# Optimization experiments

Measured on AMD Instinct MI355X. Metric: run time of the kernel, lower is better.

Reference implementation:

```python
import jax, jax.numpy as jnp
import numpy as np

B, CIN, T, H, W = 2, 512, 8, 32, 32
COUT = 512

def conv2d(x, w, b):
    # x: (B, C, H, W), w: (O, I, kh, kw) -> (B, O, H, W), SAME padding
    y = jax.lax.conv_general_dilated(x, w, (1, 1), 'SAME',
        dimension_numbers=('NCHW', 'OIHW', 'NCHW'))
    return y + b[None, :, None, None]

def convlstm(x, w, b, wci, wcf, wco):
    # x: (B, C, T, H, W) -> (B, Cout, T, H, W); peepholes wci/wcf/wco: (Cout, H, W)
    bb, c, t, hh, ww = x.shape
    cout = wci.shape[0]
    h0 = jnp.zeros((bb, cout, hh, ww), x.dtype)

    def step(carry, xt):
        Hp, Cp = carry
        z = conv2d(jnp.concatenate([xt, Hp], axis=1), w, b)  # (B, 4*Cout, H, W)
        ic, fc, cc, oc = jnp.split(z, 4, axis=1)
        i = jax.nn.sigmoid(ic + wci * Cp)
        f = jax.nn.sigmoid(fc + wcf * Cp)
        Cn = f * Cp + i * jax.nn.relu(cc)   # activation='relu'
        o = jax.nn.sigmoid(oc + wco * Cn)
        Hn = o * jax.nn.relu(Cn)
        return (Hn, Cn), Hn

    (_, _), hs = jax.lax.scan(step, (h0, h0), jnp.moveaxis(x, 2, 0))
    return jnp.moveaxis(hs, 0, 2)  # (B, Cout, T, H, W)

def setup_inputs():
    key = jax.random.key(0)
    ks = jax.random.split(key, 16)
    inp = {'x': jax.random.normal(ks[0], (B, CIN, T, H, W), jnp.float32)}
    for l in range(3):
        k = ks[1 + 5 * l: 6 + 5 * l]
        inp['conv_w%d' % (l + 1)] = jax.random.normal(k[0], (4 * COUT, CIN + COUT, 3, 3), jnp.float32) * 0.02
        inp['conv_b%d' % (l + 1)] = jnp.zeros((4 * COUT,), jnp.float32)
        inp['wci%d' % (l + 1)] = jax.random.normal(k[1], (COUT, H, W), jnp.float32) * 0.02
        inp['wcf%d' % (l + 1)] = jax.random.normal(k[2], (COUT, H, W), jnp.float32) * 0.02
        inp['wco%d' % (l + 1)] = jax.random.normal(k[3], (COUT, H, W), jnp.float32) * 0.02
    return inp

def reference(x, conv_w1, conv_b1, wci1, wcf1, wco1,
              conv_w2, conv_b2, wci2, wcf2, wco2,
              conv_w3, conv_b3, wci3, wcf3, wco3):
    y = convlstm(x, conv_w1, conv_b1, wci1, wcf1, wco1)
    y = convlstm(y, conv_w2, conv_b2, wci2, wcf2, wco2)
    y = convlstm(y, conv_w3, conv_b3, wci3, wcf3, wco3)
    # Sigmoid on last time step: output[:, :, -1] -> (B, Cout, H, W)
    return jax.nn.sigmoid(y[:, :, -1])
```

## Files before the change

kernel.cpp:

```cpp
#include <hip/hip_runtime.h>

typedef unsigned short u16;
typedef __bf16 bf16x8 __attribute__((ext_vector_type(8)));
typedef float f32x4 __attribute__((ext_vector_type(4)));

#define T_STEPS 8
#define PLANE 1156
#define ROWB 2176

__device__ __forceinline__ u16 f2bf(float f) {
    unsigned u = __float_as_uint(f);
    return (u16)((u + 0x7fff + ((u >> 16) & 1)) >> 16);
}
__device__ __forceinline__ float sigmoidf(float x) {
    return 1.f / (1.f + expf(-x));
}
__device__ __forceinline__ void gl_lds16(const void* g, void* l) {
    __builtin_amdgcn_global_load_lds(
        (const __attribute__((address_space(1))) void*)g,
        (__attribute__((address_space(3))) void*)l, 16, 0, 0);
}

__global__ __launch_bounds__(256) void repack_w(const float* __restrict__ w,
                         u16* __restrict__ wx, u16* __restrict__ wh) {
    __shared__ u16 L[128][150];
    const int tid = threadIdx.x;
    const int bidx = blockIdx.x;
    const int part   = bidx >> 9;
    const int co_blk = (bidx >> 5) & 15;
    const int cc     = (bidx >> 1) & 15;
    const int half   = bidx & 1;
    const int cibase = part * 512 + cc * 32 + half * 16;

#pragma unroll
    for (int k = 0; k < 18; ++k) {
        int i = tid + k * 256;
        int co_in = i / 36;
        int p4 = i - co_in * 36;
        int co = part ? ((co_in & 3) * 512 + co_blk * 32 + (co_in >> 2))
                      : (co_blk * 128 + co_in);
        const float4 v = *(const float4*)(w + (size_t)co * 9216
                                            + (size_t)cibase * 9 + p4 * 4);
        L[co_in][p4 * 4 + 0] = f2bf(v.x);
        L[co_in][p4 * 4 + 1] = f2bf(v.y);
        L[co_in][p4 * 4 + 2] = f2bf(v.z);
        L[co_in][p4 * 4 + 3] = f2bf(v.w);
    }
    __syncthreads();
    u16* wout = part ? wh : wx;
#pragma unroll
    for (int k = 0; k < 9; ++k) {
        int v2 = tid + k * 256;
        int co_in = v2 & 127;
        int rq = v2 >> 7;
        int q01 = rq >= 9;
        int r = rq - q01 * 9;
        int quad = half * 2 + q01;
        union { u16 u[8]; uint4 q; } tmp;
#pragma unroll
        for (int j = 0; j < 8; ++j)
            tmp.u[j] = L[co_in][(q01 * 8 + j) * 9 + r];
        *(uint4*)(wout + ((((size_t)co_blk * 144 + cc * 9 + r) * 4 + quad) * 128
                          + co_in) * 8) = tmp.q;
    }
}

__global__ __launch_bounds__(256) void pretransform_x(
    const float* __restrict__ x, u16* __restrict__ Xp) {
    const int bt = blockIdx.x >> 5;
    const int y  = blockIdx.x & 31;
    const int b  = bt >> 3;
    const int xx = threadIdx.x & 31, cg0 = threadIdx.x >> 5;
    const float* src = x + ((size_t)(b * 512) * T_STEPS + (bt & 7)) * 1024
                         + y * 32 + xx;
    u16* dst = Xp + (((size_t)bt * 34 + y + 1) * 34 + (xx + 1)) * 512;
#pragma unroll
    for (int it = 0; it < 8; ++it) {
        const int cig = cg0 + it * 8;
        union { u16 u[8]; uint4 v; } pk;
#pragma unroll
        for (int j = 0; j < 8; ++j)
            pk.u[j] = f2bf(src[(size_t)(cig * 8 + j) * 8192]);
        *(uint4*)(dst + cig * 8) = pk.v;
    }
}

#define READB4(dstv, btcp, rr) {                                             \
    const int ry_ = (rr) / 3, rx_ = (rr) % 3;                                \
    dstv[0] = *(const bf16x8*)((btcp) + wnrow + (0 + ry_) * ROWB + colb[0][rx_]); \
    dstv[1] = *(const bf16x8*)((btcp) + wnrow + (0 + ry_) * ROWB + colb[1][rx_]); \
    dstv[2] = *(const bf16x8*)((btcp) + wnrow + (1 + ry_) * ROWB + colb[0][rx_]); \
    dstv[3] = *(const bf16x8*)((btcp) + wnrow + (1 + ry_) * ROWB + colb[1][rx_]); }

#define READB2(dstv, btcp, rr) {                                             \
    const int ry_ = (rr) / 3, rx_ = (rr) % 3;                                \
    dstv[0] = *(const bf16x8*)((btcp) + wnrow + ry_ * ROWB + colb[0][rx_]);  \
    dstv[1] = *(const bf16x8*)((btcp) + wnrow + ry_ * ROWB + colb[1][rx_]); }

__global__ __launch_bounds__(512, 4) void conv_gemm(
    const u16* __restrict__ Wp, const u16* __restrict__ Xp, int t0,
    float* __restrict__ Z) {
    __shared__ __align__(16) u16 Bt[2][6528];

    const int tid = threadIdx.x;
    const int bid = blockIdx.y * 32 + blockIdx.x;
    const int swz = (bid & 7) * 64 + (bid >> 3);
    const int co_blk = swz >> 5;
    const int nblk   = swz & 31;
    const int n0 = nblk * 128;

    const int wave = tid >> 6, lane = tid & 63;
    const int wm = wave >> 1, wn = wave & 1;
    const int q_l = lane >> 4, m_l = lane & 15;

    const int plane = n0 >> 10;
    const int bb_ = plane & 1;
    const int tt  = t0 + (plane >> 1);
    const int pyb = (n0 & 1023) >> 5;
    const u16* pbase = Xp + (size_t)(bb_ * T_STEPS + tt) * PLANE * 512;

    const int c0 = tid;
    const int p0 = c0 >> 2, sl0 = c0 & 3;
    const int yl0 = p0 / 34, xl0 = p0 - yl0 * 34;
    const int src0 = ((pyb + yl0) * 34 + xl0) * 512 + ((sl0 ^ ((xl0 >> 1) & 3)) << 3);
    const int c1 = 512 + tid;
    const int p1 = c1 >> 2, sl1 = c1 & 3;
    const int yl1 = p1 / 34, xl1 = p1 - yl1 * 34;
    const int src1 = ((pyb + yl1) * 34 + xl1) * 512 + ((sl1 ^ ((xl1 >> 1) & 3)) << 3);
    const bool do1 = tid < 304;

    const uint4* Aq = (const uint4*)Wp + (size_t)co_blk * 144 * 512
                      + q_l * 128 + wm * 32 + m_l;

    int colb[2][3];
#pragma unroll
    for (int xh = 0; xh < 2; xh++)
#pragma unroll
        for (int rx = 0; rx < 3; rx++) {
            int xl = xh * 16 + m_l + rx;
            colb[xh][rx] = xl * 64 + ((q_l ^ ((xl >> 1) & 3)) << 4);
        }
    const int wnrow = wn * 2 * ROWB;

    f32x4 acc[2][4];
#pragma unroll
    for (int i = 0; i < 2; i++)
#pragma unroll
        for (int j = 0; j < 4; j++) acc[i][j] = (f32x4){0.f, 0.f, 0.f, 0.f};

    bf16x8 areg[3][2], breg[2][4];

    gl_lds16(pbase + src0, &Bt[0][c0 * 8]);
    if (do1) gl_lds16(pbase + src1, &Bt[0][c1 * 8]);
#pragma unroll
    for (int mt = 0; mt < 2; ++mt) {
        areg[0][mt] = *(const bf16x8*)(Aq + mt * 16);
        areg[1][mt] = *(const bf16x8*)(Aq + 512 + mt * 16);
    }

    for (int cc = 0; cc < 16; ++cc) {
        const int cb = cc & 1;
        const char* btc = (const char*)&Bt[cb][0];
        asm volatile("" ::: "memory");
        if (cc == 0) asm volatile("s_waitcnt vmcnt(4)" ::: "memory");
        else         asm volatile("s_waitcnt vmcnt(14)" ::: "memory");
        __builtin_amdgcn_s_barrier();
        asm volatile("" ::: "memory");
        READB4(breg[0], btc, 0);
#pragma unroll
        for (int r = 0; r < 9; ++r) {
            const int kt = cc * 9 + r;
            if (cc < 15 || r < 7) {
#pragma unroll
                for (int mt = 0; mt < 2; ++mt)
                    areg[(r + 2) % 3][mt] =
                        *(const bf16x8*)(Aq + (size_t)(kt + 2) * 512 + mt * 16);
            }
            if (r == 1 && cc < 15) {
                const u16* gs = pbase + (cc + 1) * 32;
                gl_lds16(gs + src0, &Bt[cb ^ 1][c0 * 8]);
                if (do1) gl_lds16(gs + src1, &Bt[cb ^ 1][c1 * 8]);
            }
            if (r < 8) READB4(breg[(r + 1) & 1], btc, (r + 1));
            __builtin_amdgcn_s_setprio(1);
#pragma unroll
            for (int mt = 0; mt < 2; ++mt)
#pragma unroll
                for (int nt = 0; nt < 4; ++nt)
                    acc[mt][nt] = __builtin_amdgcn_mfma_f32_16x16x32_bf16(
                        areg[r % 3][mt], breg[r & 1][nt], acc[mt][nt], 0, 0, 0);
            __builtin_amdgcn_s_setprio(0);
        }
    }

#pragma unroll
    for (int mt = 0; mt < 2; mt++)
#pragma unroll
        for (int nt = 0; nt < 4; nt++)
#pragma unroll
            for (int reg = 0; reg < 4; reg++) {
                int co = co_blk * 128 + wm * 32 + mt * 16 + q_l * 4 + reg;
                int n  = n0 + wn * 64 + nt * 16 + m_l;
                Z[(size_t)co * 4096 + n] = acc[mt][nt][reg];
            }
}

__global__ __launch_bounds__(512, 4) void hconv_gates(
    const u16* __restrict__ Wp, const u16* __restrict__ Yprev, int tprev,
    const float* __restrict__ zx, int nxoff,
    const float* __restrict__ bias,
    const float* __restrict__ wci, const float* __restrict__ wcf,
    const float* __restrict__ wco,
    float* __restrict__ C, u16* __restrict__ Yp, int t,
    float* __restrict__ outp) {
    __shared__ __align__(16) u16 Bt[2][4352];

    const int tid = threadIdx.x;
    const int bid = blockIdx.y * 32 + blockIdx.x;
    const int swz = (bid & 7) * 64 + (bid >> 3);
    const int co_blk = swz >> 5;
    const int nblk   = swz & 31;
    const int n0 = nblk * 64;

    const int wave = tid >> 6, lane = tid & 63;
    const int wm = wave >> 1, wn = wave & 1;
    const int q_l = lane >> 4, m_l = lane & 15;

    const int b = n0 >> 10;
    const int pyb = (n0 & 1023) >> 5;
    const u16* pbase = Yprev + (size_t)(b * T_STEPS + tprev) * PLANE * 512;

    const int p0 = tid >> 2, sl0 = tid & 3;
    const int yl0 = p0 / 34, xl0 = p0 - yl0 * 34;
    const int src0 = ((pyb + yl0) * 34 + xl0) * 512 + ((sl0 ^ ((xl0 >> 1) & 3)) << 3);
    const int c1 = 512 + tid;
    const int p1 = c1 >> 2, sl1 = c1 & 3;
    const int yl1 = p1 / 34, xl1 = p1 - yl1 * 34;
    const int src1 = ((pyb + yl1) * 34 + xl1) * 512 + ((sl1 ^ ((xl1 >> 1) & 3)) << 3);
    const bool do1 = tid < 32;

    const uint4* Aq = (const uint4*)Wp + (size_t)co_blk * 144 * 512
                      + q_l * 128 + wm * 32 + m_l;

    int colb[2][3];
#pragma unroll
    for (int nt = 0; nt < 2; nt++)
#pragma unroll
        for (int rx = 0; rx < 3; rx++) {
            int xl = nt * 16 + m_l + rx;
            colb[nt][rx] = xl * 64 + ((q_l ^ ((xl >> 1) & 3)) << 4);
        }
    const int wnrow = wn * ROWB;

    f32x4 acc[2][2];
#pragma unroll
    for (int i = 0; i < 2; i++)
#pragma unroll
        for (int j = 0; j < 2; j++) acc[i][j] = (f32x4){0.f, 0.f, 0.f, 0.f};

    bf16x8 areg[3][2], breg[2][2];

    gl_lds16(pbase + src0, &Bt[0][tid * 8]);
    if (do1) gl_lds16(pbase + src1, &Bt[0][c1 * 8]);
#pragma unroll
    for (int mt = 0; mt < 2; ++mt) {
        areg[0][mt] = *(const bf16x8*)(Aq + mt * 16);
        areg[1][mt] = *(const bf16x8*)(Aq + 512 + mt * 16);
    }

    for (int cc = 0; cc < 16; ++cc) {
        const int cb = cc & 1;
        const char* btc = (const char*)&Bt[cb][0];
        asm volatile("" ::: "memory");
        if (cc == 0) asm volatile("s_waitcnt vmcnt(4)" ::: "memory");
        else         asm volatile("s_waitcnt vmcnt(14)" ::: "memory");
        __builtin_amdgcn_s_barrier();
        asm volatile("" ::: "memory");
        READB2(breg[0], btc, 0);
#pragma unroll
        for (int r = 0; r < 9; ++r) {
            const int kt = cc * 9 + r;
            if (cc < 15 || r < 7) {
#pragma unroll
                for (int mt = 0; mt < 2; ++mt)
                    areg[(r + 2) % 3][mt] =
                        *(const bf16x8*)(Aq + (size_t)(kt + 2) * 512 + mt * 16);
            }
            if (r == 1 && cc < 15) {
                const u16* gs = pbase + (cc + 1) * 32;
                gl_lds16(gs + src0, &Bt[cb ^ 1][tid * 8]);
                if (do1) gl_lds16(gs + src1, &Bt[cb ^ 1][c1 * 8]);
            }
            if (r < 8) READB2(breg[(r + 1) & 1], btc, (r + 1));
            __builtin_amdgcn_s_setprio(1);
#pragma unroll
            for (int mt = 0; mt < 2; ++mt)
#pragma unroll
                for (int nt = 0; nt < 2; ++nt)
                    acc[mt][nt] = __builtin_amdgcn_mfma_f32_16x16x32_bf16(
                        areg[r % 3][mt], breg[r & 1][nt], acc[mt][nt], 0, 0, 0);
            __builtin_amdgcn_s_setprio(0);
        }
    }

#pragma unroll
    for (int mt = 0; mt < 2; ++mt) {
        const int ch = co_blk * 32 + wm * 8 + mt * 4 + q_l;
#pragma unroll
        for (int nt = 0; nt < 2; ++nt) {
            const int n = n0 + wn * 32 + nt * 16 + m_l;
            const int s = n & 1023;
            const int zcol = nxoff + n;
            float zi = acc[mt][nt][0] + zx[(size_t)ch * 4096 + zcol]          + bias[ch];
            float zf = acc[mt][nt][1] + zx[(size_t)(512 + ch) * 4096 + zcol]  + bias[512 + ch];
            float zc = acc[mt][nt][2] + zx[(size_t)(1024 + ch) * 4096 + zcol] + bias[1024 + ch];
            float zo = acc[mt][nt][3] + zx[(size_t)(1536 + ch) * 4096 + zcol] + bias[1536 + ch];
            const size_t ci_ = (size_t)(b * 512 + ch) * 1024 + s;
            const int ps = ch * 1024 + s;
            float Cp = C[ci_];
            float gi = sigmoidf(zi + wci[ps] * Cp);
            float gf = sigmoidf(zf + wcf[ps] * Cp);
            float Cn = gf * Cp + gi * fmaxf(zc, 0.f);
            float go = sigmoidf(zo + wco[ps] * Cn);
            float Hn = go * fmaxf(Cn, 0.f);
            C[ci_] = Cn;
            const int yp = (s >> 5) + 1, xp = (s & 31) + 1;
            Yp[(((size_t)(b * T_STEPS + t) * 34 + yp) * 34 + xp) * 512 + ch] = f2bf(Hn);
            if (outp) outp[ci_] = sigmoidf(Hn);
        }
    }
}

__global__ __launch_bounds__(256) void gates_kernel(
    const float* __restrict__ zx, int nxoff,
    const float* __restrict__ bias,
    const float* __restrict__ wci, const float* __restrict__ wcf,
    const float* __restrict__ wco,
    float* __restrict__ C, int is_first,
    u16* __restrict__ Yp, int t,
    float* __restrict__ outp) {
    __shared__ u16 Hs[16][136];
    const int tid = threadIdx.x;
    const int s0  = blockIdx.x * 128;
    const int co0 = blockIdx.y * 16;
    const int b   = blockIdx.z;
    const int sl = tid & 127, ch = tid >> 7;
    const int s = s0 + sl;

#pragma unroll
    for (int k = 0; k < 8; ++k) {
        const int co = co0 + k * 2 + ch;
        const size_t zi_ = (size_t)co * 4096 + nxoff + b * 1024 + s;
        float zi = zx[zi_]                       + bias[co];
        float zf = zx[zi_ + (size_t)512 * 4096]  + bias[co + 512];
        float zc = zx[zi_ + (size_t)1024 * 4096] + bias[co + 1024];
        float zo = zx[zi_ + (size_t)1536 * 4096] + bias[co + 1536];
        const size_t ci_ = ((size_t)b * 512 + co) * 1024 + s;
        float Cp = is_first ? 0.f : C[ci_];
        const int ps = co * 1024 + s;
        float gi = sigmoidf(zi + wci[ps] * Cp);
        float gf = sigmoidf(zf + wcf[ps] * Cp);
        float Cn = gf * Cp + gi * fmaxf(zc, 0.f);
        float go = sigmoidf(zo + wco[ps] * Cn);
        float Hn = go * fmaxf(Cn, 0.f);
        C[ci_] = Cn;
        Hs[k * 2 + ch][sl] = f2bf(Hn);
        if (outp) outp[ci_] = sigmoidf(Hn);
    }
    __syncthreads();
    const int sl2 = tid & 127, half = tid >> 7;
    const int s2 = s0 + sl2;
    const int yp = (s2 >> 5) + 1, xp = (s2 & 31) + 1;
    u16* dst = Yp + (((size_t)(b * T_STEPS + t) * 34 + yp) * 34 + xp) * 512
                  + co0 + half * 8;
    union { u16 u[8]; uint4 v; } pk;
#pragma unroll
    for (int j = 0; j < 8; ++j) pk.u[j] = Hs[half * 8 + j][sl2];
    *(uint4*)dst = pk.v;
}

extern "C" void kernel_launch(void* const* d_in, const int* in_sizes, int n_in,
                              void* d_out, int out_size, void* d_ws, size_t ws_size,
                              hipStream_t stream) {
    const float* x = (const float*)d_in[0];

    char* ws = (char*)d_ws;
    size_t off = 0;
    auto carve = [&](size_t bytes) { char* p = ws + off; off += (bytes + 255) & ~(size_t)255; return p; };

    u16*   Wx   = (u16*)  carve((size_t)16 * 144 * 4096 * 2);
    u16*   Wh   = (u16*)  carve((size_t)16 * 144 * 4096 * 2);
    float* Zx   = (float*)carve((size_t)2048 * 4096 * 4);
    float* Cbuf = (float*)carve((size_t)2 * 512 * 1024 * 4);
    const size_t PADB = (size_t)16 * PLANE * 512 * 2;
    u16*   Yp1  = (u16*)  carve(PADB);
    u16*   Yp2  = (u16*)  carve(PADB);
    (void)ws_size; (void)in_sizes; (void)n_in; (void)out_size;

    hipMemsetAsync(Yp1, 0, PADB, stream);
    hipMemsetAsync(Yp2, 0, PADB, stream);
    pretransform_x<<<512, 256, 0, stream>>>(x, Yp2);

    for (int l = 0; l < 3; ++l) {
        const float* w    = (const float*)d_in[1 + 5 * l];
        const float* bias = (const float*)d_in[2 + 5 * l];
        const float* wci  = (const float*)d_in[3 + 5 * l];
        const float* wcf  = (const float*)d_in[4 + 5 * l];
        const float* wco  = (const float*)d_in[5 + 5 * l];
        const u16* inl = (l == 0) ? Yp2 : (l == 1 ? Yp1 : Yp2);
        u16* Ycur      = (l == 0) ? Yp1 : (l == 1 ? Yp2 : Yp1);

        repack_w<<<1024, 256, 0, stream>>>(w, Wx, Wh);

        for (int t = 0; t < T_STEPS; ++t) {
            if ((t & 1) == 0)
                conv_gemm<<<dim3(32, 16), 512, 0, stream>>>(Wx, inl, t, Zx);
            float* outp = (l == 2 && t == T_STEPS - 1) ? (float*)d_out : nullptr;
            if (t == 0) {
                gates_kernel<<<dim3(8, 32, 2), 256, 0, stream>>>(
                    Zx, 0, bias, wci, wcf, wco, Cbuf, 1, Ycur, 0, outp);
            } else {
                hconv_gates<<<dim3(32, 16), 512, 0, stream>>>(
                    Wh, Ycur, t - 1, Zx, (t & 1) * 2048,
                    bias, wci, wcf, wco, Cbuf, Ycur, t, outp);
            }
        }
    }
}
```

Baseline: 2.075 ms.

## Deepen LDS B-fragment prefetch, unroll chunk pairs, and stage H stores through LDS

Both conv kernels now prefetch B fragments two taps ahead using a triple-buffered register set, and drop the s_setprio toggles. The 16-chunk loop is unrolled in pairs so the LDS buffer index is a compile-time constant. The gate epilogue writes bf16 H into a shared tile and then emits coalesced 16-byte stores per pixel, replacing scattered 2-byte stores. This adds register pressure and an extra barrier.

Result: slower. 2.134 ms (+2.8%).

```diff
diff --git a/kernel.cpp b/kernel.cpp
--- a/kernel.cpp
+++ b/kernel.cpp
@@ -97,6 +97,76 @@
     dstv[0] = *(const bf16x8*)((btcp) + wnrow + ry_ * ROWB + colb[0][rx_]);  \
     dstv[1] = *(const bf16x8*)((btcp) + wnrow + ry_ * ROWB + colb[1][rx_]); }
 
+#define XCHUNK(ccv, CBV)                                                      \
+{                                                                             \
+    const int cc_ = (ccv);                                                    \
+    const char* btc = (const char*)&Bt[CBV][0];                               \
+    asm volatile("" ::: "memory");                                            \
+    if (cc_ == 0) asm volatile("s_waitcnt vmcnt(4)" ::: "memory");            \
+    else          asm volatile("s_waitcnt vmcnt(14)" ::: "memory");           \
+    __builtin_amdgcn_s_barrier();                                             \
+    asm volatile("" ::: "memory");                                            \
+    READB4(breg[0], btc, 0);                                                  \
+    READB4(breg[1], btc, 1);                                                  \
+    _Pragma("unroll")                                                         \
+    for (int r = 0; r < 9; ++r) {                                             \
+        const int kt_ = cc_ * 9 + r;                                          \
+        if (cc_ < 15 || r < 7) {                                              \
+            _Pragma("unroll")                                                 \
+            for (int mt = 0; mt < 2; ++mt)                                    \
+                areg[(r + 2) % 3][mt] =                                       \
+                    *(const bf16x8*)(Aq + (size_t)(kt_ + 2) * 512 + mt * 16); \
+        }                                                                     \
+        if (r == 1 && cc_ < 15) {                                             \
+            const u16* gs = pbase + (cc_ + 1) * 32;                           \
+            gl_lds16(gs + src0, &Bt[(CBV) ^ 1][c0 * 8]);                      \
+            if (do1) gl_lds16(gs + src1, &Bt[(CBV) ^ 1][c1 * 8]);             \
+        }                                                                     \
+        if (r < 7) READB4(breg[(r + 2) % 3], btc, r + 2);                     \
+        _Pragma("unroll")                                                     \
+        for (int mt = 0; mt < 2; ++mt)                                        \
+            _Pragma("unroll")                                                 \
+            for (int nt = 0; nt < 4; ++nt)                                    \
+                acc[mt][nt] = __builtin_amdgcn_mfma_f32_16x16x32_bf16(        \
+                    areg[r % 3][mt], breg[r % 3][nt], acc[mt][nt], 0, 0, 0);  \
+    }                                                                         \
+}
+
+#define HCHUNK(ccv, CBV)                                                      \
+{                                                                             \
+    const int cc_ = (ccv);                                                    \
+    const char* btc = (const char*)&Bt[CBV][0];                               \
+    asm volatile("" ::: "memory");                                            \
+    if (cc_ == 0) asm volatile("s_waitcnt vmcnt(4)" ::: "memory");            \
+    else          asm volatile("s_waitcnt vmcnt(14)" ::: "memory");           \
+    __builtin_amdgcn_s_barrier();                                             \
+    asm volatile("" ::: "memory");                                            \
+    READB2(breg[0], btc, 0);                                                  \
+    READB2(breg[1], btc, 1);                                                  \
+    _Pragma("unroll")                                                         \
+    for (int r = 0; r < 9; ++r) {                                             \
+        const int kt_ = cc_ * 9 + r;                                          \
+        if (cc_ < 15 || r < 7) {                                              \
+            _Pragma("unroll")                                                 \
+            for (int mt = 0; mt < 2; ++mt)                                    \
+                areg[(r + 2) % 3][mt] =                                       \
+                    *(const bf16x8*)(Aq + (size_t)(kt_ + 2) * 512 + mt * 16); \
+        }                                                                     \
+        if (r == 1 && cc_ < 15) {                                             \
+            const u16* gs = pbase + (cc_ + 1) * 32;                           \
+            gl_lds16(gs + src0, &Bt[(CBV) ^ 1][tid * 8]);                     \
+            if (do1) gl_lds16(gs + src1, &Bt[(CBV) ^ 1][c1 * 8]);             \
+        }                                                                     \
+        if (r < 7) READB2(breg[(r + 2) % 3], btc, r + 2);                     \
+        _Pragma("unroll")                                                     \
+        for (int mt = 0; mt < 2; ++mt)                                        \
+            _Pragma("unroll")                                                 \
+            for (int nt = 0; nt < 2; ++nt)                                    \
+                acc[mt][nt] = __builtin_amdgcn_mfma_f32_16x16x32_bf16(        \
+                    areg[r % 3][mt], breg[r % 3][nt], acc[mt][nt], 0, 0, 0);  \
+    }                                                                         \
+}
+
 __global__ __launch_bounds__(512, 4) void conv_gemm(
     const u16* __restrict__ Wp, const u16* __restrict__ Xp, int t0,
     float* __restrict__ Z) {
@@ -148,7 +218,7 @@
 #pragma unroll
         for (int j = 0; j < 4; j++) acc[i][j] = (f32x4){0.f, 0.f, 0.f, 0.f};
 
-    bf16x8 areg[3][2], breg[2][4];
+    bf16x8 areg[3][2], breg[3][4];
 
     gl_lds16(pbase + src0, &Bt[0][c0 * 8]);
     if (do1) gl_lds16(pbase + src1, &Bt[0][c1 * 8]);
@@ -158,40 +228,13 @@
         areg[1][mt] = *(const bf16x8*)(Aq + 512 + mt * 16);
     }
 
-    for (int cc = 0; cc < 16; ++cc) {
-        const int cb = cc & 1;
-        const char* btc = (const char*)&Bt[cb][0];
-        asm volatile("" ::: "memory");
-        if (cc == 0) asm volatile("s_waitcnt vmcnt(4)" ::: "memory");
-        else         asm volatile("s_waitcnt vmcnt(14)" ::: "memory");
-        __builtin_amdgcn_s_barrier();
-        asm volatile("" ::: "memory");
-        READB4(breg[0], btc, 0);
-#pragma unroll
-        for (int r = 0; r < 9; ++r) {
-            const int kt = cc * 9 + r;
-            if (cc < 15 || r < 7) {
-#pragma unroll
-                for (int mt = 0; mt < 2; ++mt)
-                    areg[(r + 2) % 3][mt] =
-                        *(const bf16x8*)(Aq + (size_t)(kt + 2) * 512 + mt * 16);
-            }
-            if (r == 1 && cc < 15) {
-                const u16* gs = pbase + (cc + 1) * 32;
-                gl_lds16(gs + src0, &Bt[cb ^ 1][c0 * 8]);
-                if (do1) gl_lds16(gs + src1, &Bt[cb ^ 1][c1 * 8]);
-            }
-            if (r < 8) READB4(breg[(r + 1) & 1], btc, (r + 1));
-            __builtin_amdgcn_s_setprio(1);
-#pragma unroll
-            for (int mt = 0; mt < 2; ++mt)
-#pragma unroll
-                for (int nt = 0; nt < 4; ++nt)
-                    acc[mt][nt] = __builtin_amdgcn_mfma_f32_16x16x32_bf16(
-                        areg[r % 3][mt], breg[r & 1][nt], acc[mt][nt], 0, 0, 0);
-            __builtin_amdgcn_s_setprio(0);
-        }
-    }
+    XCHUNK(0, 0);
+#pragma unroll 1
+    for (int cch = 0; cch < 7; ++cch) {
+        XCHUNK(2 * cch + 1, 1);
+        XCHUNK(2 * cch + 2, 0);
+    }
+    XCHUNK(15, 1);
 
 #pragma unroll
     for (int mt = 0; mt < 2; mt++)
@@ -214,6 +257,7 @@
     float* __restrict__ C, u16* __restrict__ Yp, int t,
     float* __restrict__ outp) {
     __shared__ __align__(16) u16 Bt[2][4352];
+    __shared__ u16 Hs[32][66];
 
     const int tid = threadIdx.x;
     const int bid = blockIdx.y * 32 + blockIdx.x;
@@ -258,7 +302,7 @@
 #pragma unroll
         for (int j = 0; j < 2; j++) acc[i][j] = (f32x4){0.f, 0.f, 0.f, 0.f};
 
-    bf16x8 areg[3][2], breg[2][2];
+    bf16x8 areg[3][2], breg[3][2];
 
     gl_lds16(pbase + src0, &Bt[0][tid * 8]);
     if (do1) gl_lds16(pbase + src1, &Bt[0][c1 * 8]);
@@ -268,47 +312,22 @@
         areg[1][mt] = *(const bf16x8*)(Aq + 512 + mt * 16);
     }
 
-    for (int cc = 0; cc < 16; ++cc) {
-        const int cb = cc & 1;
-        const char* btc = (const char*)&Bt[cb][0];
-        asm volatile("" ::: "memory");
-        if (cc == 0) asm volatile("s_waitcnt vmcnt(4)" ::: "memory");
-        else         asm volatile("s_waitcnt vmcnt(14)" ::: "memory");
-        __builtin_amdgcn_s_barrier();
-        asm volatile("" ::: "memory");
-        READB2(breg[0], btc, 0);
-#pragma unroll
-        for (int r = 0; r < 9; ++r) {
-            const int kt = cc * 9 + r;
-            if (cc < 15 || r < 7) {
-#pragma unroll
-                for (int mt = 0; mt < 2; ++mt)
-                    areg[(r + 2) % 3][mt] =
-                        *(const bf16x8*)(Aq + (size_t)(kt + 2) * 512 + mt * 16);
-            }
-            if (r == 1 && cc < 15) {
-                const u16* gs = pbase + (cc + 1) * 32;
-                gl_lds16(gs + src0, &Bt[cb ^ 1][tid * 8]);
-                if (do1) gl_lds16(gs + src1, &Bt[cb ^ 1][c1 * 8]);
-            }
-            if (r < 8) READB2(breg[(r + 1) & 1], btc, (r + 1));
-            __builtin_amdgcn_s_setprio(1);
-#pragma unroll
-            for (int mt = 0; mt < 2; ++mt)
-#pragma unroll
-                for (int nt = 0; nt < 2; ++nt)
-                    acc[mt][nt] = __builtin_amdgcn_mfma_f32_16x16x32_bf16(
-                        areg[r % 3][mt], breg[r & 1][nt], acc[mt][nt], 0, 0, 0);
-            __builtin_amdgcn_s_setprio(0);
-        }
-    }
+    HCHUNK(0, 0);
+#pragma unroll 1
+    for (int cch = 0; cch < 7; ++cch) {
+        HCHUNK(2 * cch + 1, 1);
+        HCHUNK(2 * cch + 2, 0);
+    }
+    HCHUNK(15, 1);
 
 #pragma unroll
     for (int mt = 0; mt < 2; ++mt) {
-        const int ch = co_blk * 32 + wm * 8 + mt * 4 + q_l;
+        const int chl = wm * 8 + mt * 4 + q_l;
+        const int ch = co_blk * 32 + chl;
 #pragma unroll
         for (int nt = 0; nt < 2; ++nt) {
-            const int n = n0 + wn * 32 + nt * 16 + m_l;
+            const int nloc = wn * 32 + nt * 16 + m_l;
+            const int n = n0 + nloc;
             const int s = n & 1023;
             const int zcol = nxoff + n;
             float zi = acc[mt][nt][0] + zx[(size_t)ch * 4096 + zcol]          + bias[ch];
@@ -324,10 +343,20 @@
             float go = sigmoidf(zo + wco[ps] * Cn);
             float Hn = go * fmaxf(Cn, 0.f);
             C[ci_] = Cn;
-            const int yp = (s >> 5) + 1, xp = (s & 31) + 1;
-            Yp[(((size_t)(b * T_STEPS + t) * 34 + yp) * 34 + xp) * 512 + ch] = f2bf(Hn);
+            Hs[chl][nloc] = f2bf(Hn);
             if (outp) outp[ci_] = sigmoidf(Hn);
         }
+    }
+    __syncthreads();
+    if (tid < 256) {
+        const int nl = tid >> 2, cp = (tid & 3) << 3;
+        const int s = (n0 & 1023) + nl;
+        u16* yd = Yp + (((size_t)(b * T_STEPS + t) * 34 + (s >> 5) + 1) * 34
+                        + (s & 31) + 1) * 512 + co_blk * 32 + cp;
+        union { u16 u[8]; uint4 v; } pk;
+#pragma unroll
+        for (int j = 0; j < 8; ++j) pk.u[j] = Hs[cp + j][nl];
+        *(uint4*)yd = pk.v;
     }
 }
 
```

## Fuse input conv GEMM into recurrent step launch to overlap with hidden conv

Applied to the files above, without the earlier changes.

Merges the input-side conv GEMM and the recurrent hconv+gates kernel into one lstm_step kernel, selecting the role by blockIdx.z. The input conv blocks for future timesteps now run in the same launch as the recurrent work for the current step, so they can fill CUs left idle by the small recurrent grid. To make this safe the Z buffer becomes a three-slot ring (LDZ=6144 columns). The t=0 gates kernel is also simplified to drop the zero-valued cell-state terms. The cost is higher register and LDS pressure from a kernel with two branches, and contention between the two roles for bandwidth.

Measured after the change: 2.050 ms. About the same (-1.2%).

```diff
diff --git a/kernel.cpp b/kernel.cpp
--- a/kernel.cpp
+++ b/kernel.cpp
@@ -7,6 +7,7 @@
 #define T_STEPS 8
 #define PLANE 1156
 #define ROWB 2176
+#define LDZ 6144
 
 __device__ __forceinline__ u16 f2bf(float f) {
     unsigned u = __float_as_uint(f);
@@ -97,246 +98,243 @@
     dstv[0] = *(const bf16x8*)((btcp) + wnrow + ry_ * ROWB + colb[0][rx_]);  \
     dstv[1] = *(const bf16x8*)((btcp) + wnrow + ry_ * ROWB + colb[1][rx_]); }
 
-__global__ __launch_bounds__(512, 4) void conv_gemm(
-    const u16* __restrict__ Wp, const u16* __restrict__ Xp, int t0,
-    float* __restrict__ Z) {
-    __shared__ __align__(16) u16 Bt[2][6528];
-
-    const int tid = threadIdx.x;
-    const int bid = blockIdx.y * 32 + blockIdx.x;
-    const int swz = (bid & 7) * 64 + (bid >> 3);
-    const int co_blk = swz >> 5;
-    const int nblk   = swz & 31;
-    const int n0 = nblk * 128;
-
-    const int wave = tid >> 6, lane = tid & 63;
-    const int wm = wave >> 1, wn = wave & 1;
-    const int q_l = lane >> 4, m_l = lane & 15;
-
-    const int plane = n0 >> 10;
-    const int bb_ = plane & 1;
-    const int tt  = t0 + (plane >> 1);
-    const int pyb = (n0 & 1023) >> 5;
-    const u16* pbase = Xp + (size_t)(bb_ * T_STEPS + tt) * PLANE * 512;
-
-    const int c0 = tid;
-    const int p0 = c0 >> 2, sl0 = c0 & 3;
-    const int yl0 = p0 / 34, xl0 = p0 - yl0 * 34;
-    const int src0 = ((pyb + yl0) * 34 + xl0) * 512 + ((sl0 ^ ((xl0 >> 1) & 3)) << 3);
-    const int c1 = 512 + tid;
-    const int p1 = c1 >> 2, sl1 = c1 & 3;
-    const int yl1 = p1 / 34, xl1 = p1 - yl1 * 34;
-    const int src1 = ((pyb + yl1) * 34 + xl1) * 512 + ((sl1 ^ ((xl1 >> 1) & 3)) << 3);
-    const bool do1 = tid < 304;
-
-    const uint4* Aq = (const uint4*)Wp + (size_t)co_blk * 144 * 512
-                      + q_l * 128 + wm * 32 + m_l;
-
-    int colb[2][3];
-#pragma unroll
-    for (int xh = 0; xh < 2; xh++)
-#pragma unroll
-        for (int rx = 0; rx < 3; rx++) {
-            int xl = xh * 16 + m_l + rx;
-            colb[xh][rx] = xl * 64 + ((q_l ^ ((xl >> 1) & 3)) << 4);
-        }
-    const int wnrow = wn * 2 * ROWB;
-
-    f32x4 acc[2][4];
-#pragma unroll
-    for (int i = 0; i < 2; i++)
-#pragma unroll
-        for (int j = 0; j < 4; j++) acc[i][j] = (f32x4){0.f, 0.f, 0.f, 0.f};
-
-    bf16x8 areg[3][2], breg[2][4];
-
-    gl_lds16(pbase + src0, &Bt[0][c0 * 8]);
-    if (do1) gl_lds16(pbase + src1, &Bt[0][c1 * 8]);
-#pragma unroll
-    for (int mt = 0; mt < 2; ++mt) {
-        areg[0][mt] = *(const bf16x8*)(Aq + mt * 16);
-        areg[1][mt] = *(const bf16x8*)(Aq + 512 + mt * 16);
-    }
-
-    for (int cc = 0; cc < 16; ++cc) {
-        const int cb = cc & 1;
-        const char* btc = (const char*)&Bt[cb][0];
-        asm volatile("" ::: "memory");
-        if (cc == 0) asm volatile("s_waitcnt vmcnt(4)" ::: "memory");
-        else         asm volatile("s_waitcnt vmcnt(14)" ::: "memory");
-        __builtin_amdgcn_s_barrier();
-        asm volatile("" ::: "memory");
-        READB4(breg[0], btc, 0);
-#pragma unroll
-        for (int r = 0; r < 9; ++r) {
-            const int kt = cc * 9 + r;
-            if (cc < 15 || r < 7) {
-#pragma unroll
-                for (int mt = 0; mt < 2; ++mt)
-                    areg[(r + 2) % 3][mt] =
-                        *(const bf16x8*)(Aq + (size_t)(kt + 2) * 512 + mt * 16);
-            }
-            if (r == 1 && cc < 15) {
-                const u16* gs = pbase + (cc + 1) * 32;
-                gl_lds16(gs + src0, &Bt[cb ^ 1][c0 * 8]);
-                if (do1) gl_lds16(gs + src1, &Bt[cb ^ 1][c1 * 8]);
-            }
-            if (r < 8) READB4(breg[(r + 1) & 1], btc, (r + 1));
-            __builtin_amdgcn_s_setprio(1);
-#pragma unroll
-            for (int mt = 0; mt < 2; ++mt)
-#pragma unroll
-                for (int nt = 0; nt < 4; ++nt)
-                    acc[mt][nt] = __builtin_amdgcn_mfma_f32_16x16x32_bf16(
-                        areg[r % 3][mt], breg[r & 1][nt], acc[mt][nt], 0, 0, 0);
-            __builtin_amdgcn_s_setprio(0);
-        }
-    }
-
-#pragma unroll
-    for (int mt = 0; mt < 2; mt++)
-#pragma unroll
-        for (int nt = 0; nt < 4; nt++)
-#pragma unroll
-            for (int reg = 0; reg < 4; reg++) {
-                int co = co_blk * 128 + wm * 32 + mt * 16 + q_l * 4 + reg;
-                int n  = n0 + wn * 64 + nt * 16 + m_l;
-                Z[(size_t)co * 4096 + n] = acc[mt][nt][reg];
-            }
-}
-
-__global__ __launch_bounds__(512, 4) void hconv_gates(
-    const u16* __restrict__ Wp, const u16* __restrict__ Yprev, int tprev,
-    const float* __restrict__ zx, int nxoff,
+__global__ __launch_bounds__(512, 4) void lstm_step(
+    const u16* __restrict__ Wx, const u16* __restrict__ Wh,
+    const u16* __restrict__ Xp, const u16* __restrict__ Yprev,
+    int t0x, int zoffA, int zoffB,
+    int tprev, int zoffH,
     const float* __restrict__ bias,
     const float* __restrict__ wci, const float* __restrict__ wcf,
     const float* __restrict__ wco,
     float* __restrict__ C, u16* __restrict__ Yp, int t,
-    float* __restrict__ outp) {
-    __shared__ __align__(16) u16 Bt[2][4352];
+    float* __restrict__ outp,
+    float* __restrict__ Z, int role0) {
+    __shared__ __align__(16) char smem[26112];
 
     const int tid = threadIdx.x;
-    const int bid = blockIdx.y * 32 + blockIdx.x;
-    const int swz = (bid & 7) * 64 + (bid >> 3);
-    const int co_blk = swz >> 5;
-    const int nblk   = swz & 31;
-    const int n0 = nblk * 64;
-
     const int wave = tid >> 6, lane = tid & 63;
     const int wm = wave >> 1, wn = wave & 1;
     const int q_l = lane >> 4, m_l = lane & 15;
-
-    const int b = n0 >> 10;
-    const int pyb = (n0 & 1023) >> 5;
-    const u16* pbase = Yprev + (size_t)(b * T_STEPS + tprev) * PLANE * 512;
-
-    const int p0 = tid >> 2, sl0 = tid & 3;
-    const int yl0 = p0 / 34, xl0 = p0 - yl0 * 34;
-    const int src0 = ((pyb + yl0) * 34 + xl0) * 512 + ((sl0 ^ ((xl0 >> 1) & 3)) << 3);
-    const int c1 = 512 + tid;
-    const int p1 = c1 >> 2, sl1 = c1 & 3;
-    const int yl1 = p1 / 34, xl1 = p1 - yl1 * 34;
-    const int src1 = ((pyb + yl1) * 34 + xl1) * 512 + ((sl1 ^ ((xl1 >> 1) & 3)) << 3);
-    const bool do1 = tid < 32;
-
-    const uint4* Aq = (const uint4*)Wp + (size_t)co_blk * 144 * 512
-                      + q_l * 128 + wm * 32 + m_l;
-
-    int colb[2][3];
-#pragma unroll
-    for (int nt = 0; nt < 2; nt++)
-#pragma unroll
-        for (int rx = 0; rx < 3; rx++) {
-            int xl = nt * 16 + m_l + rx;
-            colb[nt][rx] = xl * 64 + ((q_l ^ ((xl >> 1) & 3)) << 4);
-        }
-    const int wnrow = wn * ROWB;
-
-    f32x4 acc[2][2];
-#pragma unroll
-    for (int i = 0; i < 2; i++)
-#pragma unroll
-        for (int j = 0; j < 2; j++) acc[i][j] = (f32x4){0.f, 0.f, 0.f, 0.f};
-
-    bf16x8 areg[3][2], breg[2][2];
-
-    gl_lds16(pbase + src0, &Bt[0][tid * 8]);
-    if (do1) gl_lds16(pbase + src1, &Bt[0][c1 * 8]);
-#pragma unroll
-    for (int mt = 0; mt < 2; ++mt) {
-        areg[0][mt] = *(const bf16x8*)(Aq + mt * 16);
-        areg[1][mt] = *(const bf16x8*)(Aq + 512 + mt * 16);
-    }
-
-    for (int cc = 0; cc < 16; ++cc) {
-        const int cb = cc & 1;
-        const char* btc = (const char*)&Bt[cb][0];
-        asm volatile("" ::: "memory");
-        if (cc == 0) asm volatile("s_waitcnt vmcnt(4)" ::: "memory");
-        else         asm volatile("s_waitcnt vmcnt(14)" ::: "memory");
-        __builtin_amdgcn_s_barrier();
-        asm volatile("" ::: "memory");
-        READB2(breg[0], btc, 0);
-#pragma unroll
-        for (int r = 0; r < 9; ++r) {
-            const int kt = cc * 9 + r;
-            if (cc < 15 || r < 7) {
+    const int bid = blockIdx.y * 32 + blockIdx.x;
+    const int swz = (bid & 7) * 64 + (bid >> 3);
+
+    if (blockIdx.z + role0 == 1) {
+        u16 (*Bt)[6528] = (u16(*)[6528])smem;
+        const int co_blk = swz >> 5;
+        const int nblk   = swz & 31;
+        const int n0 = nblk * 128;
+
+        const int plane = n0 >> 10;
+        const int bb_ = plane & 1;
+        const int tt  = t0x + (plane >> 1);
+        const int pyb = (n0 & 1023) >> 5;
+        const u16* pbase = Xp + (size_t)(bb_ * T_STEPS + tt) * PLANE * 512;
+
+        const int c0 = tid;
+        const int p0 = c0 >> 2, sl0 = c0 & 3;
+        const int yl0 = p0 / 34, xl0 = p0 - yl0 * 34;
+        const int src0 = ((pyb + yl0) * 34 + xl0) * 512 + ((sl0 ^ ((xl0 >> 1) & 3)) << 3);
+        const int c1 = 512 + tid;
+        const int p1 = c1 >> 2, sl1 = c1 & 3;
+        const int yl1 = p1 / 34, xl1 = p1 - yl1 * 34;
+        const int src1 = ((pyb + yl1) * 34 + xl1) * 512 + ((sl1 ^ ((xl1 >> 1) & 3)) << 3);
+        const bool do1 = tid < 304;
+
+        const uint4* Aq = (const uint4*)Wx + (size_t)co_blk * 144 * 512
+                          + q_l * 128 + wm * 32 + m_l;
+
+        int colb[2][3];
+#pragma unroll
+        for (int xh = 0; xh < 2; xh++)
+#pragma unroll
+            for (int rx = 0; rx < 3; rx++) {
+                int xl = xh * 16 + m_l + rx;
+                colb[xh][rx] = xl * 64 + ((q_l ^ ((xl >> 1) & 3)) << 4);
+            }
+        const int wnrow = wn * 2 * ROWB;
+
+        f32x4 acc[2][4];
+#pragma unroll
+        for (int i = 0; i < 2; i++)
+#pragma unroll
+            for (int j = 0; j < 4; j++) acc[i][j] = (f32x4){0.f, 0.f, 0.f, 0.f};
+
+        bf16x8 areg[3][2], breg[2][4];
+
+        gl_lds16(pbase + src0, &Bt[0][c0 * 8]);
+        if (do1) gl_lds16(pbase + src1, &Bt[0][c1 * 8]);
+#pragma unroll
+        for (int mt = 0; mt < 2; ++mt) {
+            areg[0][mt] = *(const bf16x8*)(Aq + mt * 16);
+            areg[1][mt] = *(const bf16x8*)(Aq + 512 + mt * 16);
+        }
+
+        for (int cc = 0; cc < 16; ++cc) {
+            const int cb = cc & 1;
+            const char* btc = (const char*)&Bt[cb][0];
+            asm volatile("" ::: "memory");
+            if (cc == 0) asm volatile("s_waitcnt vmcnt(4)" ::: "memory");
+            else         asm volatile("s_waitcnt vmcnt(14)" ::: "memory");
+            __builtin_amdgcn_s_barrier();
+            asm volatile("" ::: "memory");
+            READB4(breg[0], btc, 0);
+#pragma unroll
+            for (int r = 0; r < 9; ++r) {
+                const int kt = cc * 9 + r;
+                if (cc < 15 || r < 7) {
+#pragma unroll
+                    for (int mt = 0; mt < 2; ++mt)
+                        areg[(r + 2) % 3][mt] =
+                            *(const bf16x8*)(Aq + (size_t)(kt + 2) * 512 + mt * 16);
+                }
+                if (r == 1 && cc < 15) {
+                    const u16* gs = pbase + (cc + 1) * 32;
+                    gl_lds16(gs + src0, &Bt[cb ^ 1][c0 * 8]);
+                    if (do1) gl_lds16(gs + src1, &Bt[cb ^ 1][c1 * 8]);
+                }
+                if (r < 8) READB4(breg[(r + 1) & 1], btc, (r + 1));
+                __builtin_amdgcn_s_setprio(1);
 #pragma unroll
                 for (int mt = 0; mt < 2; ++mt)
-                    areg[(r + 2) % 3][mt] =
-                        *(const bf16x8*)(Aq + (size_t)(kt + 2) * 512 + mt * 16);
+#pragma unroll
+                    for (int nt = 0; nt < 4; ++nt)
+                        acc[mt][nt] = __builtin_amdgcn_mfma_f32_16x16x32_bf16(
+                            areg[r % 3][mt], breg[r & 1][nt], acc[mt][nt], 0, 0, 0);
+                __builtin_amdgcn_s_setprio(0);
             }
-            if (r == 1 && cc < 15) {
-                const u16* gs = pbase + (cc + 1) * 32;
-                gl_lds16(gs + src0, &Bt[cb ^ 1][tid * 8]);
-                if (do1) gl_lds16(gs + src1, &Bt[cb ^ 1][c1 * 8]);
+        }
+
+        const int zbase = ((plane >> 1) ? zoffB : zoffA) + (bb_ << 10);
+#pragma unroll
+        for (int mt = 0; mt < 2; mt++)
+#pragma unroll
+            for (int nt = 0; nt < 4; nt++)
+#pragma unroll
+                for (int reg = 0; reg < 4; reg++) {
+                    int co = co_blk * 128 + wm * 32 + mt * 16 + q_l * 4 + reg;
+                    int nlow = (n0 & 1023) + wn * 64 + nt * 16 + m_l;
+                    Z[(size_t)co * LDZ + zbase + nlow] = acc[mt][nt][reg];
+                }
+    } else {
+        u16 (*Bt)[4352] = (u16(*)[4352])smem;
+        const int co_blk = swz >> 5;
+        const int nblk   = swz & 31;
+        const int n0 = nblk * 64;
+
+        const int b = n0 >> 10;
+        const int pyb = (n0 & 1023) >> 5;
+        const u16* pbase = Yprev + (size_t)(b * T_STEPS + tprev) * PLANE * 512;
+
+        const int p0 = tid >> 2, sl0 = tid & 3;
+        const int yl0 = p0 / 34, xl0 = p0 - yl0 * 34;
+        const int src0 = ((pyb + yl0) * 34 + xl0) * 512 + ((sl0 ^ ((xl0 >> 1) & 3)) << 3);
+        const int c1 = 512 + tid;
+        const int p1 = c1 >> 2, sl1 = c1 & 3;
+        const int yl1 = p1 / 34, xl1 = p1 - yl1 * 34;
+        const int src1 = ((pyb + yl1) * 34 + xl1) * 512 + ((sl1 ^ ((xl1 >> 1) & 3)) << 3);
+        const bool do1 = tid < 32;
+
+        const uint4* Aq = (const uint4*)Wh + (size_t)co_blk * 144 * 512
+                          + q_l * 128 + wm * 32 + m_l;
+
+        int colb[2][3];
+#pragma unroll
+        for (int nt = 0; nt < 2; nt++)
+#pragma unroll
+            for (int rx = 0; rx < 3; rx++) {
+                int xl = nt * 16 + m_l + rx;
+                colb[nt][rx] = xl * 64 + ((q_l ^ ((xl >> 1) & 3)) << 4);
             }
-            if (r < 8) READB2(breg[(r + 1) & 1], btc, (r + 1));
-            __builtin_amdgcn_s_setprio(1);
-#pragma unroll
-            for (int mt = 0; mt < 2; ++mt)
-#pragma unroll
-                for (int nt = 0; nt < 2; ++nt)
-                    acc[mt][nt] = __builtin_amdgcn_mfma_f32_16x16x32_bf16(
-                        areg[r % 3][mt], breg[r & 1][nt], acc[mt][nt], 0, 0, 0);
-            __builtin_amdgcn_s_setprio(0);
-        }
-    }
-
-#pragma unroll
-    for (int mt = 0; mt < 2; ++mt) {
-        const int ch = co_blk * 32 + wm * 8 + mt * 4 + q_l;
-#pragma unroll
-        for (int nt = 0; nt < 2; ++nt) {
-            const int n = n0 + wn * 32 + nt * 16 + m_l;
-            const int s = n & 1023;
-            const int zcol = nxoff + n;
-            float zi = acc[mt][nt][0] + zx[(size_t)ch * 4096 + zcol]          + bias[ch];
-            float zf = acc[mt][nt][1] + zx[(size_t)(512 + ch) * 4096 + zcol]  + bias[512 + ch];
-            float zc = acc[mt][nt][2] + zx[(size_t)(1024 + ch) * 4096 + zcol] + bias[1024 + ch];
-            float zo = acc[mt][nt][3] + zx[(size_t)(1536 + ch) * 4096 + zcol] + bias[1536 + ch];
-            const size_t ci_ = (size_t)(b * 512 + ch) * 1024 + s;
-            const int ps = ch * 1024 + s;
-            float Cp = C[ci_];
-            float gi = sigmoidf(zi + wci[ps] * Cp);
-            float gf = sigmoidf(zf + wcf[ps] * Cp);
-            float Cn = gf * Cp + gi * fmaxf(zc, 0.f);
-            float go = sigmoidf(zo + wco[ps] * Cn);
-            float Hn = go * fmaxf(Cn, 0.f);
-            C[ci_] = Cn;
-            const int yp = (s >> 5) + 1, xp = (s & 31) + 1;
-            Yp[(((size_t)(b * T_STEPS + t) * 34 + yp) * 34 + xp) * 512 + ch] = f2bf(Hn);
-            if (outp) outp[ci_] = sigmoidf(Hn);
+        const int wnrow = wn * ROWB;
+
+        f32x4 acc[2][2];
+#pragma unroll
+        for (int i = 0; i < 2; i++)
+#pragma unroll
+            for (int j = 0; j < 2; j++) acc[i][j] = (f32x4){0.f, 0.f, 0.f, 0.f};
+
+        bf16x8 areg[3][2], breg[2][2];
+
+        gl_lds16(pbase + src0, &Bt[0][tid * 8]);
+        if (do1) gl_lds16(pbase + src1, &Bt[0][c1 * 8]);
+#pragma unroll
+        for (int mt = 0; mt < 2; ++mt) {
+            areg[0][mt] = *(const bf16x8*)(Aq + mt * 16);
+            areg[1][mt] = *(const bf16x8*)(Aq + 512 + mt * 16);
+        }
+
+        for (int cc = 0; cc < 16; ++cc) {
+            const int cb = cc & 1;
+            const char* btc = (const char*)&Bt[cb][0];
+            asm volatile("" ::: "memory");
+            if (cc == 0) asm volatile("s_waitcnt vmcnt(4)" ::: "memory");
+            else         asm volatile("s_waitcnt vmcnt(14)" ::: "memory");
+            __builtin_amdgcn_s_barrier();
+            asm volatile("" ::: "memory");
+            READB2(breg[0], btc, 0);
+#pragma unroll
+            for (int r = 0; r < 9; ++r) {
+                const int kt = cc * 9 + r;
+                if (cc < 15 || r < 7) {
+#pragma unroll
+                    for (int mt = 0; mt < 2; ++mt)
+                        areg[(r + 2) % 3][mt] =
+                            *(const bf16x8*)(Aq + (size_t)(kt + 2) * 512 + mt * 16);
+                }
+                if (r == 1 && cc < 15) {
+                    const u16* gs = pbase + (cc + 1) * 32;
+                    gl_lds16(gs + src0, &Bt[cb ^ 1][tid * 8]);
+                    if (do1) gl_lds16(gs + src1, &Bt[cb ^ 1][c1 * 8]);
+                }
+                if (r < 8) READB2(breg[(r + 1) & 1], btc, (r + 1));
+                __builtin_amdgcn_s_setprio(1);
+#pragma unroll
+                for (int mt = 0; mt < 2; ++mt)
+#pragma unroll
+                    for (int nt = 0; nt < 2; ++nt)
+                        acc[mt][nt] = __builtin_amdgcn_mfma_f32_16x16x32_bf16(
+                            areg[r % 3][mt], breg[r & 1][nt], acc[mt][nt], 0, 0, 0);
+                __builtin_amdgcn_s_setprio(0);
+            }
+        }
+
+#pragma unroll
+        for (int mt = 0; mt < 2; ++mt) {
+            const int chl = wm * 8 + mt * 4 + q_l;
+            const int ch = co_blk * 32 + chl;
+#pragma unroll
+            for (int nt = 0; nt < 2; ++nt) {
+                const int nloc = wn * 32 + nt * 16 + m_l;
+                const int n = n0 + nloc;
+                const int s = n & 1023;
+                const int zcol = zoffH + n;
+                float zi = acc[mt][nt][0] + Z[(size_t)ch * LDZ + zcol]          + bias[ch];
+                float zf = acc[mt][nt][1] + Z[(size_t)(512 + ch) * LDZ + zcol]  + bias[512 + ch];
+                float zc = acc[mt][nt][2] + Z[(size_t)(1024 + ch) * LDZ + zcol] + bias[1024 + ch];
+                float zo = acc[mt][nt][3] + Z[(size_t)(1536 + ch) * LDZ + zcol] + bias[1536 + ch];
+                const size_t ci_ = (size_t)(b * 512 + ch) * 1024 + s;
+                const int ps = ch * 1024 + s;
+                float Cp = C[ci_];
+                float gi = sigmoidf(zi + wci[ps] * Cp);
+                float gf = sigmoidf(zf + wcf[ps] * Cp);
+                float Cn = gf * Cp + gi * fmaxf(zc, 0.f);
+                float go = sigmoidf(zo + wco[ps] * Cn);
+                float Hn = go * fmaxf(Cn, 0.f);
+                C[ci_] = Cn;
+                const int yp = (s >> 5) + 1, xp = (s & 31) + 1;
+                Yp[(((size_t)(b * T_STEPS + t) * 34 + yp) * 34 + xp) * 512 + ch] = f2bf(Hn);
+                if (outp) outp[ci_] = sigmoidf(Hn);
+            }
         }
     }
 }
 
 __global__ __launch_bounds__(256) void gates_kernel(
-    const float* __restrict__ zx, int nxoff,
+    const float* __restrict__ zx,
     const float* __restrict__ bias,
     const float* __restrict__ wci, const float* __restrict__ wcf,
     const float* __restrict__ wco,
-    float* __restrict__ C, int is_first,
+    float* __restrict__ C,
     u16* __restrict__ Yp, int t,
     float* __restrict__ outp) {
     __shared__ u16 Hs[16][136];
@@ -350,19 +348,19 @@
 #pragma unroll
     for (int k = 0; k < 8; ++k) {
         const int co = co0 + k * 2 + ch;
-        const size_t zi_ = (size_t)co * 4096 + nxoff + b * 1024 + s;
-        float zi = zx[zi_]                       + bias[co];
-        float zf = zx[zi_ + (size_t)512 * 4096]  + bias[co + 512];
-        float zc = zx[zi_ + (size_t)1024 * 4096] + bias[co + 1024];
-        float zo = zx[zi_ + (size_t)1536 * 4096] + bias[co + 1536];
+        const size_t zi_ = (size_t)co * LDZ + b * 1024 + s;
+        float zi = zx[zi_]                      + bias[co];
+        float zf = zx[zi_ + (size_t)512 * LDZ]  + bias[co + 512];
+        float zc = zx[zi_ + (size_t)1024 * LDZ] + bias[co + 1024];
+        float zo = zx[zi_ + (size_t)1536 * LDZ] + bias[co + 1536];
         const size_t ci_ = ((size_t)b * 512 + co) * 1024 + s;
-        float Cp = is_first ? 0.f : C[ci_];
         const int ps = co * 1024 + s;
-        float gi = sigmoidf(zi + wci[ps] * Cp);
-        float gf = sigmoidf(zf + wcf[ps] * Cp);
-        float Cn = gf * Cp + gi * fmaxf(zc, 0.f);
+        float gi = sigmoidf(zi);
+        float gf = sigmoidf(zf);
+        float Cn = gi * fmaxf(zc, 0.f);
         float go = sigmoidf(zo + wco[ps] * Cn);
         float Hn = go * fmaxf(Cn, 0.f);
+        (void)gf; (void)wci; (void)wcf;
         C[ci_] = Cn;
         Hs[k * 2 + ch][sl] = f2bf(Hn);
         if (outp) outp[ci_] = sigmoidf(Hn);
@@ -390,7 +388,7 @@
 
     u16*   Wx   = (u16*)  carve((size_t)16 * 144 * 4096 * 2);
     u16*   Wh   = (u16*)  carve((size_t)16 * 144 * 4096 * 2);
-    float* Zx   = (float*)carve((size_t)2048 * 4096 * 4);
+    float* Zx   = (float*)carve((size_t)2048 * LDZ * 4);
     float* Cbuf = (float*)carve((size_t)2 * 512 * 1024 * 4);
     const size_t PADB = (size_t)16 * PLANE * 512 * 2;
     u16*   Yp1  = (u16*)  carve(PADB);
@@ -412,18 +410,23 @@
 
         repack_w<<<1024, 256, 0, stream>>>(w, Wx, Wh);
 
-        for (int t = 0; t < T_STEPS; ++t) {
-            if ((t & 1) == 0)
-                conv_gemm<<<dim3(32, 16), 512, 0, stream>>>(Wx, inl, t, Zx);
+        lstm_step<<<dim3(32, 16, 1), 512, 0, stream>>>(
+            Wx, Wh, inl, Ycur, 0, 0, 2048,
+            0, 0, bias, wci, wcf, wco,
+            Cbuf, Ycur, 0, nullptr, Zx, 1);
+        gates_kernel<<<dim3(8, 32, 2), 256, 0, stream>>>(
+            Zx, bias, wci, wcf, wco, Cbuf, Ycur, 0, nullptr);
+
+        for (int t = 1; t < T_STEPS; ++t) {
+            const bool fuse = (t == 1 || t == 3 || t == 5);
             float* outp = (l == 2 && t == T_STEPS - 1) ? (float*)d_out : nullptr;
-            if (t == 0) {
-                gates_kernel<<<dim3(8, 32, 2), 256, 0, stream>>>(
-                    Zx, 0, bias, wci, wcf, wco, Cbuf, 1, Ycur, 0, outp);
-            } else {
-                hconv_gates<<<dim3(32, 16), 512, 0, stream>>>(
-                    Wh, Ycur, t - 1, Zx, (t & 1) * 2048,
-                    bias, wci, wcf, wco, Cbuf, Ycur, t, outp);
-            }
-        }
-    }
-}
+            const int zoffH = (t % 3) * 2048;
+            const int zA = ((t + 1) % 3) * 2048;
+            const int zB = ((t + 2) % 3) * 2048;
+            lstm_step<<<dim3(32, 16, fuse ? 2 : 1), 512, 0, stream>>>(
+                Wx, Wh, inl, Ycur, t + 1, zA, zB,
+                t - 1, zoffH, bias, wci, wcf, wco,
+                Cbuf, Ycur, t, outp, Zx, 0);
+        }
+    }
+}
```
